# Kernel optimization log

Hardware: AMD Instinct MI355X
Metric: run time of the kernel (lower is better)

Reference implementation:

```python
import jax, jax.numpy as jnp
import numpy as np

N = 100000
E = 400000
NFEAT, NHID, NOUT, NHEAD = 128, 64, 128, 4
HIDDEN = NHID * NHEAD  # 256
SLOPE = 0.2


def gat_conv(x, src, dst, W, a_src, a_dst, b, concat):
    """PyG-style GATConv (eval mode, self-loops already appended to src/dst).
    x: [N, Fin]; W: [Fin, H*C]; a_src/a_dst: [H, C]; b: [H*C] or [C]."""
    H, C = a_src.shape
    h = (x @ W).reshape(N, H, C)                      # [N,H,C]
    al_s = (h * a_src).sum(-1)                        # [N,H] per-node src score
    al_d = (h * a_dst).sum(-1)                        # [N,H] per-node dst score
    e = jax.nn.leaky_relu(al_s[src] + al_d[dst], SLOPE)  # [Et,H]
    # segment softmax over incoming edges of each dst node
    m = jax.ops.segment_max(e, dst, num_segments=N)
    m = jnp.where(jnp.isfinite(m), m, 0.0)
    ex = jnp.exp(e - m[dst])
    denom = jax.ops.segment_sum(ex, dst, num_segments=N)
    alpha = ex / (denom[dst] + 1e-16)                 # [Et,H]
    msg = alpha[:, :, None] * h[src]                  # [Et,H,C]
    out = jax.ops.segment_sum(msg, dst, num_segments=N)  # [N,H,C]
    out = out.reshape(N, H * C) if concat else out.mean(axis=1)
    return out + b


def setup_inputs() -> dict:
    key = jax.random.key(0)
    ks = jax.random.split(key, 16)
    x = jax.random.normal(ks[0], (N, NFEAT), dtype=jnp.float32)
    edge_index = jax.random.randint(ks[1], (2, E), 0, N, dtype=jnp.int64)
    s = 0.1
    inp = {
        'x': x, 'edge_index': edge_index,
        # layer 0: nfeat -> nhid x nhead (concat)
        'W0': jax.random.normal(ks[2], (NFEAT, HIDDEN), jnp.float32) * s,
        'as0': jax.random.normal(ks[3], (NHEAD, NHID), jnp.float32) * s,
        'ad0': jax.random.normal(ks[4], (NHEAD, NHID), jnp.float32) * s,
        'b0': jnp.zeros((HIDDEN,), jnp.float32),
        # layer 1: hidden -> nhid x nhead (concat)
        'W1': jax.random.normal(ks[5], (HIDDEN, HIDDEN), jnp.float32) * s,
        'as1': jax.random.normal(ks[6], (NHEAD, NHID), jnp.float32) * s,
        'ad1': jax.random.normal(ks[7], (NHEAD, NHID), jnp.float32) * s,
        'b1': jnp.zeros((HIDDEN,), jnp.float32),
        # output layer: hidden -> nout, heads=1, concat=False
        'W2': jax.random.normal(ks[8], (HIDDEN, NOUT), jnp.float32) * s,
        'as2': jax.random.normal(ks[9], (1, NOUT), jnp.float32) * s,
        'ad2': jax.random.normal(ks[10], (1, NOUT), jnp.float32) * s,
        'b2': jnp.zeros((NOUT,), jnp.float32),
    }
    return inp


def reference(x, edge_index, W0, as0, ad0, b0, W1, as1, ad1, b1, W2, as2, ad2, b2):
    # PyG GATConv adds self-loops by default; edge set is shared across layers.
    loop = jnp.arange(N, dtype=edge_index.dtype)
    src = jnp.concatenate([edge_index[0], loop])
    dst = jnp.concatenate([edge_index[1], loop])
    # dropout inactive in eval mode
    h = jax.nn.elu(gat_conv(x, src, dst, W0, as0, ad0, b0, concat=True))
    h = jax.nn.elu(gat_conv(h, src, dst, W1, as1, ad1, b1, concat=True))
    out = gat_conv(h, src, dst, W2, as2, ad2, b2, concat=False)
    return out
```

## Files before the change

### kernel.cpp

```cpp
#include <hip/hip_runtime.h>
#include <cmath>

#define NN 100000
#define EE 400000
#define ET (EE + NN)
#define SLOPE 0.2f

typedef __attribute__((ext_vector_type(8))) short short8;
typedef __attribute__((ext_vector_type(4))) float floatx4;

__device__ __forceinline__ float b2f(ushort u) {
    union { unsigned int i; float f; } v; v.i = ((unsigned int)u) << 16; return v.f;
}
__device__ __forceinline__ ushort f2b(float f) {
    union { float f; unsigned int i; } v; v.f = f;
    unsigned int r = v.i + 0x7FFFu + ((v.i >> 16) & 1u);
    return (ushort)(r >> 16);
}

__global__ __launch_bounds__(256) void count_deg(const int* __restrict__ ei, int* __restrict__ deg) {
    int e = blockIdx.x * 256 + threadIdx.x;
    if (e < EE) atomicAdd(&deg[ei[EE + e]], 1);
}

__global__ __launch_bounds__(256) void scan1(const int* __restrict__ deg, int* __restrict__ incl,
                                             int* __restrict__ bsums) {
    __shared__ int ts[256];
    int b = blockIdx.x, t = threadIdx.x;
    int base = b * 1024 + t * 4;
    int v[4];
#pragma unroll
    for (int i = 0; i < 4; i++) {
        int n = base + i;
        v[i] = (n < NN) ? (deg[n] + 1) : 0;
    }
    int s = 0;
#pragma unroll
    for (int i = 0; i < 4; i++) { s += v[i]; v[i] = s; }
    ts[t] = s;
    __syncthreads();
    for (int off = 1; off < 256; off <<= 1) {
        int x = (t >= off) ? ts[t - off] : 0;
        __syncthreads();
        ts[t] += x;
        __syncthreads();
    }
    int excl = ts[t] - s;
#pragma unroll
    for (int i = 0; i < 4; i++) {
        int n = base + i;
        if (n < NN) incl[n] = v[i] + excl;
    }
    if (t == 255) bsums[b] = ts[255];
}

__global__ __launch_bounds__(128) void scan2(int* __restrict__ bsums, int nblk) {
    __shared__ int ts[128];
    int t = threadIdx.x;
    int v = (t < nblk) ? bsums[t] : 0;
    ts[t] = v;
    __syncthreads();
    for (int off = 1; off < 128; off <<= 1) {
        int x = (t >= off) ? ts[t - off] : 0;
        __syncthreads();
        ts[t] += x;
        __syncthreads();
    }
    if (t < nblk) bsums[t] = ts[t] - v;
}

__global__ __launch_bounds__(256) void scan3(const int* __restrict__ incl, const int* __restrict__ deg,
                                             const int* __restrict__ bsums, int* __restrict__ row_ptr,
                                             int* __restrict__ cursor) {
    int n = blockIdx.x * 256 + threadIdx.x;
    if (n < NN) {
        int rp = incl[n] - (deg[n] + 1) + bsums[n >> 10];
        row_ptr[n] = rp;
        cursor[n] = rp;
    }
    if (n == 0) row_ptr[NN] = ET;
}

__global__ __launch_bounds__(256) void scatter(const int* __restrict__ ei, int* __restrict__ cursor,
                                               int* __restrict__ col) {
    int e = blockIdx.x * 256 + threadIdx.x;
    if (e < EE) {
        int d = ei[EE + e];
        int p = atomicAdd(&cursor[d], 1);
        col[p] = ei[e];
    }
}

__global__ __launch_bounds__(256) void selfloop(const int* __restrict__ cursor, int* __restrict__ col) {
    int n = blockIdx.x * 256 + threadIdx.x;
    if (n < NN) col[cursor[n]] = n;
}

__global__ __launch_bounds__(256) void cast_to_bf16(const float* __restrict__ in,
                                                    ushort* __restrict__ out, int n4) {
    int i = blockIdx.x * 256 + threadIdx.x;
    if (i < n4) {
        float4 v = ((const float4*)in)[i];
        ushort4 o;
        o.x = f2b(v.x); o.y = f2b(v.y); o.z = f2b(v.z); o.w = f2b(v.w);
        ((ushort4*)out)[i] = o;
    }
}

__global__ __launch_bounds__(256) void transpose_cast(const float* __restrict__ W,
                                                      ushort* __restrict__ Wt, int K, int N) {
    int idx = blockIdx.x * 256 + threadIdx.x;
    if (idx < N * K) {
        int n = idx / K, k = idx % K;
        Wt[idx] = f2b(W[(size_t)k * N + n]);
    }
}

#define LP 40
__global__ __launch_bounds__(256) void gemm_bf16(const ushort* __restrict__ A,
                                                 const ushort* __restrict__ Bt,
                                                 ushort* __restrict__ C,
                                                 int M, int K, int N) {
    __shared__ ushort As[128 * LP];
    __shared__ ushort Bs[128 * LP];
    int tid = threadIdx.x;
    int bm = blockIdx.x * 128;
    int bn = blockIdx.y * 128;
    int wave = tid >> 6, lane = tid & 63;
    int wm = (wave >> 1) * 64, wn = (wave & 1) * 64;

    floatx4 acc[4][4];
#pragma unroll
    for (int i = 0; i < 4; i++)
#pragma unroll
        for (int j = 0; j < 4; j++) acc[i][j] = (floatx4)0.f;

    int r = tid >> 1;
    int c = (tid & 1) * 16;

    int frow = lane & 15;
    int kq = (lane >> 4) * 8;

    for (int k0 = 0; k0 < K; k0 += 32) {
        uint4 a0, a1;
        if (bm + r < M) {
            const uint4* ap = (const uint4*)(A + (size_t)(bm + r) * K + k0 + c);
            a0 = ap[0]; a1 = ap[1];
        } else {
            a0 = make_uint4(0, 0, 0, 0); a1 = a0;
        }
        *(uint4*)&As[r * LP + c]     = a0;
        *(uint4*)&As[r * LP + c + 8] = a1;

        const uint4* bp = (const uint4*)(Bt + (size_t)(bn + r) * K + k0 + c);
        *(uint4*)&Bs[r * LP + c]     = bp[0];
        *(uint4*)&Bs[r * LP + c + 8] = bp[1];

        __syncthreads();

        short8 afr[4], bfr[4];
#pragma unroll
        for (int i = 0; i < 4; i++)
            afr[i] = *(const short8*)&As[(wm + i * 16 + frow) * LP + kq];
#pragma unroll
        for (int j = 0; j < 4; j++)
            bfr[j] = *(const short8*)&Bs[(wn + j * 16 + frow) * LP + kq];
#pragma unroll
        for (int i = 0; i < 4; i++)
#pragma unroll
            for (int j = 0; j < 4; j++)
                acc[i][j] = __builtin_amdgcn_mfma_f32_16x16x32_bf16(afr[i], bfr[j], acc[i][j], 0, 0, 0);

        __syncthreads();
    }

    int ccol = bn + wn + (lane & 15);
    int crow = bm + wm + (lane >> 4) * 4;
#pragma unroll
    for (int i = 0; i < 4; i++) {
#pragma unroll
        for (int reg = 0; reg < 4; reg++) {
            int row = crow + i * 16 + reg;
            if (row < M) {
#pragma unroll
                for (int j = 0; j < 4; j++)
                    C[(size_t)row * N + ccol + j * 16] = f2b(acc[i][j][reg]);
            }
        }
    }
}

template <int H, int HC>
__global__ __launch_bounds__(256) void scores_k(const ushort* __restrict__ h,
                                                const float* __restrict__ a_s,
                                                const float* __restrict__ a_d,
                                                float* __restrict__ als,
                                                float* __restrict__ ald) {
    constexpr int CP = HC / 64;
    constexpr int GS = 64 / H;
    int wv = threadIdx.x >> 6, lane = threadIdx.x & 63;
    int n = blockIdx.x * 4 + wv;
    if (n >= NN) return;
    const uint* p = (const uint*)(h + (size_t)n * HC + lane * CP);
    float s = 0.f, d = 0.f;
#pragma unroll
    for (int q = 0; q < CP / 2; q++) {
        uint u = p[q];
        int ch = lane * CP + 2 * q;
        float v0 = b2f((ushort)(u & 0xffff)), v1 = b2f((ushort)(u >> 16));
        s += v0 * a_s[ch] + v1 * a_s[ch + 1];
        d += v0 * a_d[ch] + v1 * a_d[ch + 1];
    }
#pragma unroll
    for (int off = 1; off < GS; off <<= 1) {
        s += __shfl_xor(s, off, 64);
        d += __shfl_xor(d, off, 64);
    }
    if ((lane & (GS - 1)) == 0) {
        int head = lane / GS;
        als[n * H + head] = s;
        ald[n * H + head] = d;
    }
}

template <int H, int HC, bool ELU_ACT, bool OUT_BF16>
__global__ __launch_bounds__(256) void aggregate(const ushort* __restrict__ hlin,
                                                 const float* __restrict__ als,
                                                 const float* __restrict__ ald,
                                                 const int* __restrict__ row_ptr,
                                                 const int* __restrict__ col,
                                                 const float* __restrict__ bias,
                                                 void* __restrict__ outv) {
    constexpr int CP = HC / 64;
    constexpr int GS = 64 / H;
    int wv = threadIdx.x >> 6, lane = threadIdx.x & 63;
    int dst = blockIdx.x * 4 + wv;
    if (dst >= NN) return;
    int rs = row_ptr[dst], re = row_ptr[dst + 1];
    int deg = re - rs;
    int eg = lane & (GS - 1);
    int head = lane / GS;
    float ad = ald[dst * H + head];

    float acc[CP];
#pragma unroll
    for (int j = 0; j < CP; j++) acc[j] = 0.f;

    uint laneoff = (uint)(lane * CP);

    if (deg <= GS) {
        int src = 0;
        float s = -1e30f;
        if (eg < deg) {
            src = col[rs + eg];
            float sc = als[src * H + head] + ad;
            s = sc > 0.f ? sc : SLOPE * sc;
        }
        float m = s;
#pragma unroll
        for (int off = 1; off < GS; off <<= 1) m = fmaxf(m, __shfl_xor(m, off, 64));
        float e = (eg < deg) ? __expf(s - m) : 0.f;
        float sum = e;
#pragma unroll
        for (int off = 1; off < GS; off <<= 1) sum += __shfl_xor(sum, off, 64);
        float w = e * (1.0f / (sum + 1e-16f));

        int hbase = head * GS;
        int d = 0;
        for (; d + 4 <= deg; d += 4) {
            int s0 = __shfl(src, d, 64),     s1 = __shfl(src, d + 1, 64);
            int s2 = __shfl(src, d + 2, 64), s3 = __shfl(src, d + 3, 64);
            float w0 = __shfl(w, hbase + d, 64),     w1 = __shfl(w, hbase + d + 1, 64);
            float w2 = __shfl(w, hbase + d + 2, 64), w3 = __shfl(w, hbase + d + 3, 64);
            const uint* p0 = (const uint*)(hlin + (uint)s0 * HC + laneoff);
            const uint* p1 = (const uint*)(hlin + (uint)s1 * HC + laneoff);
            const uint* p2 = (const uint*)(hlin + (uint)s2 * HC + laneoff);
            const uint* p3 = (const uint*)(hlin + (uint)s3 * HC + laneoff);
            uint u0[CP / 2], u1[CP / 2], u2[CP / 2], u3[CP / 2];
#pragma unroll
            for (int q = 0; q < CP / 2; q++) { u0[q] = p0[q]; u1[q] = p1[q]; u2[q] = p2[q]; u3[q] = p3[q]; }
#pragma unroll
            for (int q = 0; q < CP / 2; q++) {
                acc[2*q]   += w0 * b2f((ushort)(u0[q] & 0xffff)) + w1 * b2f((ushort)(u1[q] & 0xffff))
                            + w2 * b2f((ushort)(u2[q] & 0xffff)) + w3 * b2f((ushort)(u3[q] & 0xffff));
                acc[2*q+1] += w0 * b2f((ushort)(u0[q] >> 16)) + w1 * b2f((ushort)(u1[q] >> 16))
                            + w2 * b2f((ushort)(u2[q] >> 16)) + w3 * b2f((ushort)(u3[q] >> 16));
            }
        }
        for (; d < deg; d++) {
            int sd = __shfl(src, d, 64);
            float wd = __shfl(w, hbase + d, 64);
            const uint* p = (const uint*)(hlin + (uint)sd * HC + laneoff);
#pragma unroll
            for (int q = 0; q < CP / 2; q++) {
                uint u = p[q];
                acc[2*q]   += wd * b2f((ushort)(u & 0xffff));
                acc[2*q+1] += wd * b2f((ushort)(u >> 16));
            }
        }
    } else {
        float m = -1e30f;
        for (int e2 = eg; e2 < deg; e2 += GS) {
            int sc0 = col[rs + e2];
            float sc = als[sc0 * H + head] + ad;
            sc = sc > 0.f ? sc : SLOPE * sc;
            m = fmaxf(m, sc);
        }
#pragma unroll
        for (int off = 1; off < GS; off <<= 1) m = fmaxf(m, __shfl_xor(m, off, 64));
        float sum = 0.f;
        for (int e2 = eg; e2 < deg; e2 += GS) {
            int sc0 = col[rs + e2];
            float sc = als[sc0 * H + head] + ad;
            sc = sc > 0.f ? sc : SLOPE * sc;
            sum += __expf(sc - m);
        }
#pragma unroll
        for (int off = 1; off < GS; off <<= 1) sum += __shfl_xor(sum, off, 64);
        float inv = 1.0f / (sum + 1e-16f);
        for (int d = 0; d < deg; d++) {
            int sd = col[rs + d];
            float sc = als[sd * H + head] + ad;
            sc = sc > 0.f ? sc : SLOPE * sc;
            float wd = __expf(sc - m) * inv;
            const uint* p = (const uint*)(hlin + (uint)sd * HC + laneoff);
#pragma unroll
            for (int q = 0; q < CP / 2; q++) {
                uint u = p[q];
                acc[2*q]   += wd * b2f((ushort)(u & 0xffff));
                acc[2*q+1] += wd * b2f((ushort)(u >> 16));
            }
        }
    }

#pragma unroll
    for (int j = 0; j < CP; j++) {
        float v = acc[j] + bias[lane * CP + j];
        if (ELU_ACT) v = v > 0.f ? v : (__expf(v) - 1.0f);
        acc[j] = v;
    }
    if (OUT_BF16) {
        ushort* outp = (ushort*)outv + (size_t)dst * HC + laneoff;
        uint pk[CP / 2];
#pragma unroll
        for (int q = 0; q < CP / 2; q++)
            pk[q] = (uint)f2b(acc[2*q]) | ((uint)f2b(acc[2*q+1]) << 16);
#pragma unroll
        for (int q = 0; q < CP / 2; q++) ((uint*)outp)[q] = pk[q];
    } else {
        float* outp = (float*)outv + (size_t)dst * HC + laneoff;
#pragma unroll
        for (int j = 0; j < CP; j++) outp[j] = acc[j];
    }
}

extern "C" void kernel_launch(void* const* d_in, const int* in_sizes, int n_in,
                              void* d_out, int out_size, void* d_ws, size_t ws_size,
                              hipStream_t stream) {
    const float* x   = (const float*)d_in[0];
    const int*   ei  = (const int*)d_in[1];
    const float* W0  = (const float*)d_in[2];
    const float* as0 = (const float*)d_in[3];
    const float* ad0 = (const float*)d_in[4];
    const float* b0  = (const float*)d_in[5];
    const float* W1  = (const float*)d_in[6];
    const float* as1 = (const float*)d_in[7];
    const float* ad1 = (const float*)d_in[8];
    const float* b1  = (const float*)d_in[9];
    const float* W2  = (const float*)d_in[10];
    const float* as2 = (const float*)d_in[11];
    const float* ad2 = (const float*)d_in[12];
    const float* b2  = (const float*)d_in[13];
    float* out = (float*)d_out;

    char* ws = (char*)d_ws;
    size_t off = 0;
    auto alloc = [&](size_t bytes) {
        void* p = ws + off;
        off += (bytes + 255) & ~(size_t)255;
        return p;
    };
    ushort* xb   = (ushort*)alloc((size_t)NN * 128 * 2);
    ushort* h    = (ushort*)alloc((size_t)NN * 256 * 2);
    ushort* actB = (ushort*)alloc((size_t)NN * 256 * 2);
    ushort* actC = (ushort*)alloc((size_t)NN * 256 * 2);
    ushort* Wt0  = (ushort*)alloc((size_t)256 * 128 * 2);
    ushort* Wt1  = (ushort*)alloc((size_t)256 * 256 * 2);
    ushort* Wt2  = (ushort*)alloc((size_t)128 * 256 * 2);
    float* als   = (float*)alloc((size_t)NN * 4 * 4);
    float* ald   = (float*)alloc((size_t)NN * 4 * 4);
    int* deg     = (int*)alloc((size_t)NN * 4);
    int* incl    = (int*)alloc((size_t)NN * 4);
    int* row_ptr = (int*)alloc((size_t)(NN + 1) * 4);
    int* cursor  = (int*)alloc((size_t)NN * 4);
    int* col     = (int*)alloc((size_t)ET * 4);
    int* bsums   = (int*)alloc(128 * 4);

    const int NBLK = (NN + 1023) / 1024;

    hipMemsetAsync(deg, 0, (size_t)NN * 4, stream);
    count_deg<<<(EE + 255) / 256, 256, 0, stream>>>(ei, deg);
    scan1<<<NBLK, 256, 0, stream>>>(deg, incl, bsums);
    scan2<<<1, 128, 0, stream>>>(bsums, NBLK);
    scan3<<<(NN + 255) / 256, 256, 0, stream>>>(incl, deg, bsums, row_ptr, cursor);
    scatter<<<(EE + 255) / 256, 256, 0, stream>>>(ei, cursor, col);
    selfloop<<<(NN + 255) / 256, 256, 0, stream>>>(cursor, col);

    cast_to_bf16<<<(NN * 128 / 4 + 255) / 256, 256, 0, stream>>>(x, xb, NN * 128 / 4);
    transpose_cast<<<(256 * 128 + 255) / 256, 256, 0, stream>>>(W0, Wt0, 128, 256);
    transpose_cast<<<(256 * 256 + 255) / 256, 256, 0, stream>>>(W1, Wt1, 256, 256);
    transpose_cast<<<(128 * 256 + 255) / 256, 256, 0, stream>>>(W2, Wt2, 256, 128);

    const int GM = (NN + 127) / 128;
    const int NB4 = (NN + 3) / 4;

    gemm_bf16<<<dim3(GM, 2), 256, 0, stream>>>(xb, Wt0, h, NN, 128, 256);
    scores_k<4, 256><<<NB4, 256, 0, stream>>>(h, as0, ad0, als, ald);
    aggregate<4, 256, true, true><<<NB4, 256, 0, stream>>>(h, als, ald, row_ptr, col, b0, actB);

    gemm_bf16<<<dim3(GM, 2), 256, 0, stream>>>(actB, Wt1, h, NN, 256, 256);
    scores_k<4, 256><<<NB4, 256, 0, stream>>>(h, as1, ad1, als, ald);
    aggregate<4, 256, true, true><<<NB4, 256, 0, stream>>>(h, als, ald, row_ptr, col, b1, actC);

    gemm_bf16<<<dim3(GM, 1), 256, 0, stream>>>(actC, Wt2, h, NN, 256, 128);
    scores_k<1, 128><<<NB4, 256, 0, stream>>>(h, as2, ad2, als, ald);
    aggregate<1, 128, false, false><<<NB4, 256, 0, stream>>>(h, als, ald, row_ptr, col, b2, out);
}
```

Measured before the change: 470.8 us.

## Fuse attention score computation into GEMM epilogue and process two nodes per wave

Attention score dot products (h·a_src, h·a_dst) are now computed in the GEMM epilogue from the fp32 accumulators, so the separate scores kernel and its re-read of h go away. The output layer uses atomics into zeroed buffers because its single head spans two waves. The aggregation kernel now handles two destination nodes per wave using half-waves, to improve lane utilisation for low-degree nodes. The three weight transposes are merged into one launch. Risks: scores are now taken from fp32 values rather than the bf16-rounded h, the half-waves diverge when the two nodes differ in degree, and the grid assumes NN divisible by 8.

```diff
diff --git a/kernel.cpp b/kernel.cpp
--- a/kernel.cpp
+++ b/kernel.cpp
@@ -11,6 +11,12 @@
 
 __device__ __forceinline__ float b2f(ushort u) {
     union { unsigned int i; float f; } v; v.i = ((unsigned int)u) << 16; return v.f;
+}
+__device__ __forceinline__ float bl(uint u) {
+    union { unsigned int i; float f; } v; v.i = u << 16; return v.f;
+}
+__device__ __forceinline__ float bh(uint u) {
+    union { unsigned int i; float f; } v; v.i = u & 0xffff0000u; return v.f;
 }
 __device__ __forceinline__ ushort f2b(float f) {
     union { float f; unsigned int i; } v; v.f = f;
@@ -107,12 +113,24 @@
     }
 }
 
-__global__ __launch_bounds__(256) void transpose_cast(const float* __restrict__ W,
-                                                      ushort* __restrict__ Wt, int K, int N) {
+__global__ __launch_bounds__(256) void transpose_cast_all(const float* __restrict__ W0,
+                                                          const float* __restrict__ W1,
+                                                          const float* __restrict__ W2,
+                                                          ushort* __restrict__ Wt0,
+                                                          ushort* __restrict__ Wt1,
+                                                          ushort* __restrict__ Wt2) {
     int idx = blockIdx.x * 256 + threadIdx.x;
-    if (idx < N * K) {
-        int n = idx / K, k = idx % K;
-        Wt[idx] = f2b(W[(size_t)k * N + n]);
+    if (idx < 32768) {
+        int n = idx >> 7, k = idx & 127;
+        Wt0[idx] = f2b(W0[(size_t)k * 256 + n]);
+    } else if (idx < 32768 + 65536) {
+        int j = idx - 32768;
+        int n = j >> 8, k = j & 255;
+        Wt1[j] = f2b(W1[(size_t)k * 256 + n]);
+    } else if (idx < 131072) {
+        int j = idx - 98304;
+        int n = j >> 8, k = j & 255;
+        Wt2[j] = f2b(W2[(size_t)k * 128 + n]);
     }
 }
 
@@ -120,7 +138,12 @@
 __global__ __launch_bounds__(256) void gemm_bf16(const ushort* __restrict__ A,
                                                  const ushort* __restrict__ Bt,
                                                  ushort* __restrict__ C,
-                                                 int M, int K, int N) {
+                                                 int M, int K, int N,
+                                                 const float* __restrict__ asf,
+                                                 const float* __restrict__ adf,
+                                                 float* __restrict__ als,
+                                                 float* __restrict__ ald,
+                                                 int H, int lgC) {
     __shared__ ushort As[128 * LP];
     __shared__ ushort Bs[128 * LP];
     int tid = threadIdx.x;
@@ -188,65 +211,70 @@
             }
         }
     }
-}
-
-template <int H, int HC>
-__global__ __launch_bounds__(256) void scores_k(const ushort* __restrict__ h,
-                                                const float* __restrict__ a_s,
-                                                const float* __restrict__ a_d,
-                                                float* __restrict__ als,
-                                                float* __restrict__ ald) {
-    constexpr int CP = HC / 64;
-    constexpr int GS = 64 / H;
+
+    {
+        int cb = bn + wn + (lane & 15);
+        float asv[4], adv[4];
+#pragma unroll
+        for (int j = 0; j < 4; j++) {
+            asv[j] = asf[cb + j * 16];
+            adv[j] = adf[cb + j * 16];
+        }
+        int hidx = (bn + wn) >> lgC;
+#pragma unroll
+        for (int i = 0; i < 4; i++) {
+#pragma unroll
+            for (int reg = 0; reg < 4; reg++) {
+                float ss = acc[i][0][reg] * asv[0] + acc[i][1][reg] * asv[1]
+                         + acc[i][2][reg] * asv[2] + acc[i][3][reg] * asv[3];
+                float dd = acc[i][0][reg] * adv[0] + acc[i][1][reg] * adv[1]
+                         + acc[i][2][reg] * adv[2] + acc[i][3][reg] * adv[3];
+#pragma unroll
+                for (int off = 1; off < 16; off <<= 1) {
+                    ss += __shfl_xor(ss, off, 64);
+                    dd += __shfl_xor(dd, off, 64);
+                }
+                int row = crow + i * 16 + reg;
+                if ((lane & 15) == 0 && row < M) {
+                    if (lgC == 6) {
+                        als[row * H + hidx] = ss;
+                        ald[row * H + hidx] = dd;
+                    } else {
+                        atomicAdd(&als[row], ss);
+                        atomicAdd(&ald[row], dd);
+                    }
+                }
+            }
+        }
+    }
+}
+
+template <int H, int HC, bool ELU_ACT, bool OUT_BF16>
+__global__ __launch_bounds__(256) void aggregate2(const ushort* __restrict__ hlin,
+                                                  const float* __restrict__ als,
+                                                  const float* __restrict__ ald,
+                                                  const int* __restrict__ row_ptr,
+                                                  const int* __restrict__ col,
+                                                  const float* __restrict__ bias,
+                                                  void* __restrict__ outv) {
+    constexpr int CP = HC / 32;
+    constexpr int GS = 32 / H;
+    constexpr int NU = CP / 2;
     int wv = threadIdx.x >> 6, lane = threadIdx.x & 63;
-    int n = blockIdx.x * 4 + wv;
-    if (n >= NN) return;
-    const uint* p = (const uint*)(h + (size_t)n * HC + lane * CP);
-    float s = 0.f, d = 0.f;
-#pragma unroll
-    for (int q = 0; q < CP / 2; q++) {
-        uint u = p[q];
-        int ch = lane * CP + 2 * q;
-        float v0 = b2f((ushort)(u & 0xffff)), v1 = b2f((ushort)(u >> 16));
-        s += v0 * a_s[ch] + v1 * a_s[ch + 1];
-        d += v0 * a_d[ch] + v1 * a_d[ch + 1];
-    }
-#pragma unroll
-    for (int off = 1; off < GS; off <<= 1) {
-        s += __shfl_xor(s, off, 64);
-        d += __shfl_xor(d, off, 64);
-    }
-    if ((lane & (GS - 1)) == 0) {
-        int head = lane / GS;
-        als[n * H + head] = s;
-        ald[n * H + head] = d;
-    }
-}
-
-template <int H, int HC, bool ELU_ACT, bool OUT_BF16>
-__global__ __launch_bounds__(256) void aggregate(const ushort* __restrict__ hlin,
-                                                 const float* __restrict__ als,
-                                                 const float* __restrict__ ald,
-                                                 const int* __restrict__ row_ptr,
-                                                 const int* __restrict__ col,
-                                                 const float* __restrict__ bias,
-                                                 void* __restrict__ outv) {
-    constexpr int CP = HC / 64;
-    constexpr int GS = 64 / H;
-    int wv = threadIdx.x >> 6, lane = threadIdx.x & 63;
-    int dst = blockIdx.x * 4 + wv;
-    if (dst >= NN) return;
-    int rs = row_ptr[dst], re = row_ptr[dst + 1];
-    int deg = re - rs;
-    int eg = lane & (GS - 1);
-    int head = lane / GS;
+    int hl = lane & 31;
+    int dst = blockIdx.x * 8 + wv * 2 + (lane >> 5);
+    int rs = row_ptr[dst];
+    int deg = row_ptr[dst + 1] - rs;
+    int eg = hl & (GS - 1);
+    int head = hl / GS;
     float ad = ald[dst * H + head];
+    uint uoff = (uint)hl * NU;
 
     float acc[CP];
 #pragma unroll
     for (int j = 0; j < CP; j++) acc[j] = 0.f;
 
-    uint laneoff = (uint)(lane * CP);
+    int degB = __shfl_xor(deg, 32, 64);
 
     if (deg <= GS) {
         int src = 0;
@@ -265,44 +293,37 @@
         for (int off = 1; off < GS; off <<= 1) sum += __shfl_xor(sum, off, 64);
         float w = e * (1.0f / (sum + 1e-16f));
 
-        int hbase = head * GS;
-        int d = 0;
-        for (; d + 4 <= deg; d += 4) {
-            int s0 = __shfl(src, d, 64),     s1 = __shfl(src, d + 1, 64);
-            int s2 = __shfl(src, d + 2, 64), s3 = __shfl(src, d + 3, 64);
-            float w0 = __shfl(w, hbase + d, 64),     w1 = __shfl(w, hbase + d + 1, 64);
-            float w2 = __shfl(w, hbase + d + 2, 64), w3 = __shfl(w, hbase + d + 3, 64);
-            const uint* p0 = (const uint*)(hlin + (uint)s0 * HC + laneoff);
-            const uint* p1 = (const uint*)(hlin + (uint)s1 * HC + laneoff);
-            const uint* p2 = (const uint*)(hlin + (uint)s2 * HC + laneoff);
-            const uint* p3 = (const uint*)(hlin + (uint)s3 * HC + laneoff);
-            uint u0[CP / 2], u1[CP / 2], u2[CP / 2], u3[CP / 2];
-#pragma unroll
-            for (int q = 0; q < CP / 2; q++) { u0[q] = p0[q]; u1[q] = p1[q]; u2[q] = p2[q]; u3[q] = p3[q]; }
-#pragma unroll
-            for (int q = 0; q < CP / 2; q++) {
-                acc[2*q]   += w0 * b2f((ushort)(u0[q] & 0xffff)) + w1 * b2f((ushort)(u1[q] & 0xffff))
-                            + w2 * b2f((ushort)(u2[q] & 0xffff)) + w3 * b2f((ushort)(u3[q] & 0xffff));
-                acc[2*q+1] += w0 * b2f((ushort)(u0[q] >> 16)) + w1 * b2f((ushort)(u1[q] >> 16))
-                            + w2 * b2f((ushort)(u2[q] >> 16)) + w3 * b2f((ushort)(u3[q] >> 16));
-            }
-        }
-        for (; d < deg; d++) {
-            int sd = __shfl(src, d, 64);
-            float wd = __shfl(w, hbase + d, 64);
-            const uint* p = (const uint*)(hlin + (uint)sd * HC + laneoff);
-#pragma unroll
-            for (int q = 0; q < CP / 2; q++) {
-                uint u = p[q];
-                acc[2*q]   += wd * b2f((ushort)(u & 0xffff));
-                acc[2*q+1] += wd * b2f((ushort)(u >> 16));
+        int mdeg = max(deg, (degB <= GS) ? degB : 0);
+        int sbase = lane & 32;
+        int wbase = (lane & 32) | (hl & ~(GS - 1));
+
+        for (int d = 0; d < mdeg; d += 4) {
+            int s0 = __shfl(src, sbase + d, 64);
+            int s1 = __shfl(src, sbase + d + 1, 64);
+            int s2 = __shfl(src, sbase + d + 2, 64);
+            int s3 = __shfl(src, sbase + d + 3, 64);
+            float w0 = __shfl(w, wbase + d, 64);
+            float w1 = __shfl(w, wbase + d + 1, 64);
+            float w2 = __shfl(w, wbase + d + 2, 64);
+            float w3 = __shfl(w, wbase + d + 3, 64);
+            const uint* p0 = (const uint*)(hlin + (size_t)s0 * HC) + uoff;
+            const uint* p1 = (const uint*)(hlin + (size_t)s1 * HC) + uoff;
+            const uint* p2 = (const uint*)(hlin + (size_t)s2 * HC) + uoff;
+            const uint* p3 = (const uint*)(hlin + (size_t)s3 * HC) + uoff;
+            uint u0[NU], u1[NU], u2[NU], u3[NU];
+#pragma unroll
+            for (int q = 0; q < NU; q++) { u0[q] = p0[q]; u1[q] = p1[q]; u2[q] = p2[q]; u3[q] = p3[q]; }
+#pragma unroll
+            for (int q = 0; q < NU; q++) {
+                acc[2*q]   += w0 * bl(u0[q]) + w1 * bl(u1[q]) + w2 * bl(u2[q]) + w3 * bl(u3[q]);
+                acc[2*q+1] += w0 * bh(u0[q]) + w1 * bh(u1[q]) + w2 * bh(u2[q]) + w3 * bh(u3[q]);
             }
         }
     } else {
         float m = -1e30f;
         for (int e2 = eg; e2 < deg; e2 += GS) {
-            int sc0 = col[rs + e2];
-            float sc = als[sc0 * H + head] + ad;
+            int s0 = col[rs + e2];
+            float sc = als[s0 * H + head] + ad;
             sc = sc > 0.f ? sc : SLOPE * sc;
             m = fmaxf(m, sc);
         }
@@ -310,8 +331,8 @@
         for (int off = 1; off < GS; off <<= 1) m = fmaxf(m, __shfl_xor(m, off, 64));
         float sum = 0.f;
         for (int e2 = eg; e2 < deg; e2 += GS) {
-            int sc0 = col[rs + e2];
-            float sc = als[sc0 * H + head] + ad;
+            int s0 = col[rs + e2];
+            float sc = als[s0 * H + head] + ad;
             sc = sc > 0.f ? sc : SLOPE * sc;
             sum += __expf(sc - m);
         }
@@ -323,32 +344,32 @@
             float sc = als[sd * H + head] + ad;
             sc = sc > 0.f ? sc : SLOPE * sc;
             float wd = __expf(sc - m) * inv;
-            const uint* p = (const uint*)(hlin + (uint)sd * HC + laneoff);
-#pragma unroll
-            for (int q = 0; q < CP / 2; q++) {
+            const uint* p = (const uint*)(hlin + (size_t)sd * HC) + uoff;
+#pragma unroll
+            for (int q = 0; q < NU; q++) {
                 uint u = p[q];
-                acc[2*q]   += wd * b2f((ushort)(u & 0xffff));
-                acc[2*q+1] += wd * b2f((ushort)(u >> 16));
+                acc[2*q]   += wd * bl(u);
+                acc[2*q+1] += wd * bh(u);
             }
         }
     }
 
 #pragma unroll
     for (int j = 0; j < CP; j++) {
-        float v = acc[j] + bias[lane * CP + j];
+        float v = acc[j] + bias[hl * CP + j];
         if (ELU_ACT) v = v > 0.f ? v : (__expf(v) - 1.0f);
         acc[j] = v;
     }
     if (OUT_BF16) {
-        ushort* outp = (ushort*)outv + (size_t)dst * HC + laneoff;
-        uint pk[CP / 2];
-#pragma unroll
-        for (int q = 0; q < CP / 2; q++)
+        uint* outp = (uint*)((ushort*)outv + (size_t)dst * HC) + uoff;
+        uint pk[NU];
+#pragma unroll
+        for (int q = 0; q < NU; q++)
             pk[q] = (uint)f2b(acc[2*q]) | ((uint)f2b(acc[2*q+1]) << 16);
 #pragma unroll
-        for (int q = 0; q < CP / 2; q++) ((uint*)outp)[q] = pk[q];
+        for (int q = 0; q < NU; q++) outp[q] = pk[q];
     } else {
-        float* outp = (float*)outv + (size_t)dst * HC + laneoff;
+        float* outp = (float*)outv + (size_t)dst * HC + hl * CP;
 #pragma unroll
         for (int j = 0; j < CP; j++) outp[j] = acc[j];
     }
@@ -407,22 +428,19 @@
     selfloop<<<(NN + 255) / 256, 256, 0, stream>>>(cursor, col);
 
     cast_to_bf16<<<(NN * 128 / 4 + 255) / 256, 256, 0, stream>>>(x, xb, NN * 128 / 4);
-    transpose_cast<<<(256 * 128 + 255) / 256, 256, 0, stream>>>(W0, Wt0, 128, 256);
-    transpose_cast<<<(256 * 256 + 255) / 256, 256, 0, stream>>>(W1, Wt1, 256, 256);
-    transpose_cast<<<(128 * 256 + 255) / 256, 256, 0, stream>>>(W2, Wt2, 256, 128);
+    transpose_cast_all<<<(131072 + 255) / 256, 256, 0, stream>>>(W0, W1, W2, Wt0, Wt1, Wt2);
 
     const int GM = (NN + 127) / 128;
-    const int NB4 = (NN + 3) / 4;
-
-    gemm_bf16<<<dim3(GM, 2), 256, 0, stream>>>(xb, Wt0, h, NN, 128, 256);
-    scores_k<4, 256><<<NB4, 256, 0, stream>>>(h, as0, ad0, als, ald);
-    aggregate<4, 256, true, true><<<NB4, 256, 0, stream>>>(h, als, ald, row_ptr, col, b0, actB);
-
-    gemm_bf16<<<dim3(GM, 2), 256, 0, stream>>>(actB, Wt1, h, NN, 256, 256);
-    scores_k<4, 256><<<NB4, 256, 0, stream>>>(h, as1, ad1, als, ald);
-    aggregate<4, 256, true, true><<<NB4, 256, 0, stream>>>(h, als, ald, row_ptr, col, b1, actC);
-
-    gemm_bf16<<<dim3(GM, 1), 256, 0, stream>>>(actC, Wt2, h, NN, 256, 128);
-    scores_k<1, 128><<<NB4, 256, 0, stream>>>(h, as2, ad2, als, ald);
-    aggregate<1, 128, false, false><<<NB4, 256, 0, stream>>>(h, als, ald, row_ptr, col, b2, out);
-}
+    const int NB8 = NN / 8;
+
+    gemm_bf16<<<dim3(GM, 2), 256, 0, stream>>>(xb, Wt0, h, NN, 128, 256, as0, ad0, als, ald, 4, 6);
+    aggregate2<4, 256, true, true><<<NB8, 256, 0, stream>>>(h, als, ald, row_ptr, col, b0, actB);
+
+    gemm_bf16<<<dim3(GM, 2), 256, 0, stream>>>(actB, Wt1, h, NN, 256, 256, as1, ad1, als, ald, 4, 6);
+    aggregate2<4, 256, true, true><<<NB8, 256, 0, stream>>>(h, als, ald, row_ptr, col, b1, actC);
+
+    hipMemsetAsync(als, 0, (size_t)NN * 4, stream);
+    hipMemsetAsync(ald, 0, (size_t)NN * 4, stream);
+    gemm_bf16<<<dim3(GM, 1), 256, 0, stream>>>(actC, Wt2, h, NN, 256, 128, as2, ad2, als, ald, 1, 7);
+    aggregate2<1, 128, false, false><<<NB8, 256, 0, stream>>>(h, als, ald, row_ptr, col, b2, out);
+}
```

Measured after the change: 441.8 us. 1.07x faster.
